# Optimization experiments

Measured on AMD Instinct MI355X. Metric: run time of the kernel, lower is better.

## Reference

```python
import jax, jax.numpy as jnp
import numpy as np

VOCAB = 32000; DIM = 512; NL = 6; B = 2; L = 1024
DI = 2 * DIM      # d_inner (expand=2)
DS = 16           # d_state
DC = 4            # d_conv
DR = DIM // 16    # dt_rank = ceil(512/16) = 32


def setup_inputs() -> dict:
    key = jax.random.key(0)
    ks = jax.random.split(key, 10)
    s = 0.02
    tokens = jax.random.randint(ks[0], (B, L), 0, VOCAB)
    pos_emb = jax.random.normal(ks[1], (1, L, DIM)) * s
    embed = jax.random.normal(ks[2], (VOCAB, DIM)) * s
    lm_w = jax.random.normal(ks[3], (VOCAB, DIM)) * s
    lm_b = jnp.zeros((VOCAB,), jnp.float32)
    in_proj_w = jax.random.normal(ks[4], (NL, 2 * DI, DIM)) * s
    conv_w = jax.random.normal(ks[5], (NL, DI, DC)) * s
    conv_b = jnp.zeros((NL, DI), jnp.float32)
    x_proj_w = jax.random.normal(ks[6], (NL, DR + 2 * DS, DI)) * s
    dt_proj_w = jax.random.normal(ks[7], (NL, DI, DR)) * s
    dt_proj_b = jnp.broadcast_to(jnp.log(jnp.expm1(jnp.float32(0.01))), (NL, DI)).astype(jnp.float32)
    A_log = jnp.log(jnp.broadcast_to(jnp.arange(1, DS + 1, dtype=jnp.float32), (NL, DI, DS)))
    Dp = jnp.ones((NL, DI), jnp.float32)
    out_w = jax.random.normal(ks[8], (NL, DIM, DI)) * s
    ln_g = jnp.ones((NL, DIM), jnp.float32)
    ln_b = jnp.zeros((NL, DIM), jnp.float32)
    return dict(tokens=tokens, pos_emb=pos_emb, embed=embed, lm_w=lm_w, lm_b=lm_b,
                in_proj_w=in_proj_w, conv_w=conv_w, conv_b=conv_b, x_proj_w=x_proj_w,
                dt_proj_w=dt_proj_w, dt_proj_b=dt_proj_b, A_log=A_log, Dp=Dp,
                out_w=out_w, ln_g=ln_g, ln_b=ln_b)


def silu(x):
    return x * jax.nn.sigmoid(x)


def layernorm(x, g, b, eps=1e-5):
    mu = jnp.mean(x, -1, keepdims=True)
    var = jnp.var(x, -1, keepdims=True)
    return (x - mu) * jax.lax.rsqrt(var + eps) * g + b


def causal_dwconv(x, w, b):
    # x: (B,L,DI), w: (DI,DC) depthwise, left-pad causal
    xp = jnp.pad(x, ((0, 0), (DC - 1, 0), (0, 0)))
    y = b
    for k in range(DC):
        y = y + w[:, k] * xp[:, k:k + x.shape[1], :]
    return y


def selective_scan(u, dt, A, Bm, Cm, Dp):
    # u,dt: (B,L,DI); A: (DI,DS); Bm,Cm: (B,L,DS)
    dA = jnp.exp(dt[..., None] * A)                       # (B,L,DI,DS)
    dBu = dt[..., None] * Bm[:, :, None, :] * u[..., None]
    h0 = jnp.zeros((u.shape[0], DI, DS), u.dtype)

    def step(h, inp):
        dA_t, dBu_t, C_t = inp
        h = dA_t * h + dBu_t
        y = jnp.einsum('bdn,bn->bd', h, C_t)
        return h, y

    _, ys = jax.lax.scan(step, h0, (dA.transpose(1, 0, 2, 3),
                                    dBu.transpose(1, 0, 2, 3),
                                    Cm.transpose(1, 0, 2)))
    return ys.transpose(1, 0, 2) + u * Dp


def mamba_block(x, in_w, cw, cb, xp_w, dtw, dtb, A_log, Dp, ow):
    xz = jnp.einsum('bld,ed->ble', x, in_w)               # (B,L,2*DI)
    xc, z = jnp.split(xz, 2, axis=-1)
    xc = silu(causal_dwconv(xc, cw, cb))
    x_dbl = jnp.einsum('bld,ed->ble', xc, xp_w)           # (B,L,DR+2*DS)
    dt, Bm, Cm = jnp.split(x_dbl, [DR, DR + DS], axis=-1)
    dt = jax.nn.softplus(jnp.einsum('blr,dr->bld', dt, dtw) + dtb)
    A = -jnp.exp(A_log)
    y = selective_scan(xc, dt, A, Bm, Cm, Dp)
    y = y * silu(z)
    return jnp.einsum('bld,ed->ble', y, ow)


def reference(tokens, pos_emb, embed, lm_w, lm_b, in_proj_w, conv_w, conv_b,
              x_proj_w, dt_proj_w, dt_proj_b, A_log, Dp, out_w, ln_g, ln_b):
    x = embed[tokens] + pos_emb[:, :tokens.shape[1]]
    for i in range(NL):
        res = x
        x = mamba_block(x, in_proj_w[i], conv_w[i], conv_b[i], x_proj_w[i],
                        dt_proj_w[i], dt_proj_b[i], A_log[i], Dp[i], out_w[i])
        x = layernorm(x + res, ln_g[i], ln_b[i])
    return jnp.einsum('bld,vd->blv', x, lm_w) + lm_b
```

## Files before the change

### kernel.cpp

```cpp
#include <hip/hip_runtime.h>
#include <hip/hip_bf16.h>
#include <math.h>

#define BB 2
#define LL 1024
#define DIM 512
#define NL 6
#define DI 1024
#define DS 16
#define DC 4
#define DR 32
#define VOCAB 32000
#define M_ROWS (BB * LL)
#define CCH 64
#define CHLEN (LL / CCH)
#define KSPLIT 8
#define OSPLIT 4

typedef unsigned short u16;
typedef __attribute__((ext_vector_type(8))) short bf16x8;
typedef __attribute__((ext_vector_type(4))) float f32x4;

__device__ __forceinline__ u16 f2bf(float f) {
    unsigned u = __float_as_uint(f);
    u += 0x7FFF + ((u >> 16) & 1);
    return (u16)(u >> 16);
}
__device__ __forceinline__ float bf2f(u16 h) {
    return __uint_as_float(((unsigned)h) << 16);
}
#define SWZ(r, c) ((c) ^ (((r) >> 1) & 3))

__global__ __launch_bounds__(256) void cast_all(const float* __restrict__ lm,
                                                const float* __restrict__ inw,
                                                const float* __restrict__ ow,
                                                const float* __restrict__ xp,
                                                u16* __restrict__ lmb,
                                                u16* __restrict__ inb,
                                                u16* __restrict__ owb_,
                                                u16* __restrict__ xpb) {
    int idx = blockIdx.x * 256 + threadIdx.x;
    const float* src; u16* dst; int off;
    if (idx < 2048000)      { src = lm;  dst = lmb;  off = idx; }
    else if (idx < 2834432) { src = inw; dst = inb;  off = idx - 2048000; }
    else if (idx < 3227648) { src = ow;  dst = owb_; off = idx - 2834432; }
    else                    { src = xp;  dst = xpb;  off = idx - 3227648; }
    float4 v0 = ((const float4*)src)[off * 2];
    float4 v1 = ((const float4*)src)[off * 2 + 1];
    union { u16 h[8]; int4 v; } r;
    r.h[0] = f2bf(v0.x); r.h[1] = f2bf(v0.y); r.h[2] = f2bf(v0.z); r.h[3] = f2bf(v0.w);
    r.h[4] = f2bf(v1.x); r.h[5] = f2bf(v1.y); r.h[6] = f2bf(v1.z); r.h[7] = f2bf(v1.w);
    ((int4*)dst)[off] = r.v;
}

__global__ __launch_bounds__(256) void embed_kernel(const int* __restrict__ tok,
                                                    const float* __restrict__ pos,
                                                    const float* __restrict__ emb,
                                                    float* __restrict__ x,
                                                    u16* __restrict__ xb) {
    int idx = blockIdx.x * 256 + threadIdx.x;
    int d = idx & (DIM - 1);
    int l = (idx >> 9) & (LL - 1);
    int b = idx >> 19;
    int t = tok[b * LL + l];
    float v = emb[(size_t)t * DIM + d] + pos[l * DIM + d];
    x[idx] = v;
    xb[idx] = f2bf(v);
}

__global__ __launch_bounds__(256) void gemm_n64(const u16* __restrict__ A,
                                                const u16* __restrict__ W,
                                                float* __restrict__ out,
                                                u16* __restrict__ outb,
                                                const float* __restrict__ bias,
                                                int lda, int ldw, int ldc,
                                                int KS, int pstride) {
    __shared__ __align__(16) char smem_raw[24576];
    u16* As = (u16*)smem_raw;
    u16* Ws = (u16*)(smem_raw + 16384);
    float* Cs = (float*)smem_raw;

    const int t = threadIdx.x;
    const int l = t & 63;
    const int w = t >> 6;
    const int gx = gridDim.x, gy = gridDim.y;
    const int nwg = gx * gy * gridDim.z;
    const int fid = (blockIdx.z * gy + blockIdx.y) * gx + blockIdx.x;
    const int q8 = nwg >> 3, r8 = nwg & 7;
    const int xcd = fid & 7, rank = fid >> 3;
    const int wgid = (xcd < r8 ? xcd * (q8 + 1) : r8 * (q8 + 1) + (xcd - r8) * q8) + rank;
    const int kz = wgid % gx;
    const int bm = ((wgid / gx) % gy) * 128;
    const int bnn = (wgid / (gx * gy)) * 64;
    const int wm = w * 32;

    f32x4 acc[2][4] = {};
    const int nt = KS >> 5;
    const int kbeg = kz * KS;

    auto STAGE = [&](int bufi, int k0) {
#pragma unroll
        for (int p = 0; p < 2; ++p) {
            const int i = p * 256 + w * 64 + l;
            const int row = i >> 2;
            const int kq = SWZ(row, i & 3);
            __builtin_amdgcn_global_load_lds(
                (const __attribute__((address_space(1))) unsigned int*)
                    (A + (size_t)(bm + row) * lda + k0 + kq * 8),
                (__attribute__((address_space(3))) unsigned int*)
                    (As + bufi * 4096 + (p * 256 + w * 64) * 8),
                16, 0, 0);
        }
        {
            const int i = w * 64 + l;
            const int row = i >> 2;
            const int kq = SWZ(row, i & 3);
            __builtin_amdgcn_global_load_lds(
                (const __attribute__((address_space(1))) unsigned int*)
                    (W + (size_t)(bnn + row) * ldw + k0 + kq * 8),
                (__attribute__((address_space(3))) unsigned int*)
                    (Ws + bufi * 2048 + (w * 64) * 8),
                16, 0, 0);
        }
    };
    auto COMPUTE = [&](int bufi) {
        const u16* Ab = As + bufi * 4096;
        const u16* Wb = Ws + bufi * 2048;
        bf16x8 bfr[4];
#pragma unroll
        for (int ni = 0; ni < 4; ++ni) {
            const int wr = ni * 16 + (l & 15);
            bfr[ni] = *(const bf16x8*)(Wb + wr * 32 + SWZ(wr, l >> 4) * 8);
        }
#pragma unroll
        for (int mi = 0; mi < 2; ++mi) {
            const int ar = wm + mi * 16 + (l & 15);
            bf16x8 a = *(const bf16x8*)(Ab + ar * 32 + SWZ(ar, l >> 4) * 8);
#pragma unroll
            for (int ni = 0; ni < 4; ++ni)
                acc[mi][ni] = __builtin_amdgcn_mfma_f32_16x16x32_bf16(bfr[ni], a, acc[mi][ni], 0, 0, 0);
        }
    };

    STAGE(0, kbeg);
    for (int tt = 0; tt < nt; ++tt) {
        if (tt + 1 < nt) {
            STAGE((tt + 1) & 1, kbeg + ((tt + 1) << 5));
            asm volatile("s_waitcnt vmcnt(3)\ns_barrier" ::: "memory");
        } else {
            asm volatile("s_waitcnt vmcnt(0)\ns_barrier" ::: "memory");
        }
        COMPUTE(tt & 1);
        asm volatile("s_waitcnt lgkmcnt(0)\ns_barrier" ::: "memory");
    }

    if (outb != nullptr) {
        u16* opb = outb + (size_t)kz * pstride;
#pragma unroll
        for (int mi = 0; mi < 2; ++mi) {
            const int row = bm + wm + mi * 16 + (l & 15);
#pragma unroll
            for (int ni = 0; ni < 4; ++ni) {
                const int col = bnn + ni * 16 + ((l >> 4) << 2);
                ushort4 v;
                v.x = f2bf(acc[mi][ni][0]); v.y = f2bf(acc[mi][ni][1]);
                v.z = f2bf(acc[mi][ni][2]); v.w = f2bf(acc[mi][ni][3]);
                *(ushort4*)(opb + (size_t)row * ldc + col) = v;
            }
        }
    } else {
        float* op = out + (size_t)kz * pstride;
#pragma unroll
        for (int pass = 0; pass < 2; ++pass) {
            if ((w >> 1) == pass) {
                const int rbase = (w & 1) * 32;
#pragma unroll
                for (int mi = 0; mi < 2; ++mi) {
                    const int r = rbase + mi * 16 + (l & 15);
#pragma unroll
                    for (int ni = 0; ni < 4; ++ni) {
                        const int c = ni * 16 + ((l >> 4) << 2);
                        float4 v;
                        v.x = acc[mi][ni][0]; v.y = acc[mi][ni][1];
                        v.z = acc[mi][ni][2]; v.w = acc[mi][ni][3];
                        *(float4*)(Cs + r * 65 + c) = v;
                    }
                }
            }
            __syncthreads();
#pragma unroll
            for (int it = 0; it < 4; ++it) {
                const int idx = it * 256 + t;
                const int r = idx >> 4;
                const int c4 = (idx & 15) * 4;
                float4 v = *(float4*)(Cs + r * 65 + c4);
                if (bias != nullptr) {
                    float4 b4 = *(const float4*)(bias + bnn + c4);
                    v.x += b4.x; v.y += b4.y; v.z += b4.z; v.w += b4.w;
                }
                *(float4*)(op + (size_t)(bm + pass * 64 + r) * ldc + bnn + c4) = v;
            }
            __syncthreads();
        }
    }
}

__global__ __launch_bounds__(256) void conv_silu(const u16* __restrict__ xzb,
                                                 const float* __restrict__ cw,
                                                 const float* __restrict__ cb,
                                                 u16* __restrict__ xcb) {
    int idx8 = blockIdx.x * 256 + threadIdx.x;
    int c0 = (idx8 & 127) * 8;
    int m = idx8 >> 7;
    int l = m & (LL - 1);

    float acc[8];
    float4 cb0 = *(const float4*)(cb + c0);
    float4 cb1 = *(const float4*)(cb + c0 + 4);
    acc[0] = cb0.x; acc[1] = cb0.y; acc[2] = cb0.z; acc[3] = cb0.w;
    acc[4] = cb1.x; acc[5] = cb1.y; acc[6] = cb1.z; acc[7] = cb1.w;
#pragma unroll
    for (int k = 0; k < DC; ++k) {
        int ll = l + k - (DC - 1);
        if (ll < 0) continue;
        const u16* row = xzb + ((size_t)(m + k - (DC - 1))) * (2 * DI) + c0;
        ushort4 r0 = *(const ushort4*)row;
        ushort4 r1 = *(const ushort4*)(row + 4);
#pragma unroll
        for (int j = 0; j < 4; ++j) {
            acc[j]     += cw[(c0 + j) * DC + k]     * bf2f(((const u16*)&r0)[j]);
            acc[j + 4] += cw[(c0 + j + 4) * DC + k] * bf2f(((const u16*)&r1)[j]);
        }
    }
    ushort4 o0, o1;
#pragma unroll
    for (int j = 0; j < 4; ++j) {
        float v0 = acc[j]     / (1.f + __expf(-acc[j]));
        float v1 = acc[j + 4] / (1.f + __expf(-acc[j + 4]));
        ((u16*)&o0)[j] = f2bf(v0);
        ((u16*)&o1)[j] = f2bf(v1);
    }
    u16* op = xcb + (size_t)idx8 * 8;
    *(ushort4*)op = o0;
    *(ushort4*)(op + 4) = o1;
}

__global__ __launch_bounds__(256) void scan_pass1(const u16* __restrict__ xcb,
                                                  const float* __restrict__ Pf,
                                                  const float* __restrict__ dtw,
                                                  const float* __restrict__ dtb,
                                                  const float* __restrict__ A_log,
                                                  float* __restrict__ S,
                                                  float* __restrict__ Q) {
    __shared__ float xds[CHLEN][64];
    const int t = threadIdx.x;
    const int d = blockIdx.x * 256 + t;
    const int b = blockIdx.y;
    const int c = blockIdx.z;
    const int l0 = c * CHLEN;
    const int m0 = b * LL + l0;

    for (int i = t; i < CHLEN * 64; i += 256) {
        int r = i >> 6, cc = i & 63;
        float s = 0.f;
#pragma unroll
        for (int kz = 0; kz < KSPLIT; ++kz)
            s += Pf[(size_t)kz * (M_ROWS * 64) + (m0 + r) * 64 + cc];
        xds[r][cc] = s;
    }
    __syncthreads();

    float4 wreg[8];
#pragma unroll
    for (int kk = 0; kk < 8; ++kk)
        wreg[kk] = *(const float4*)(dtw + (size_t)d * DR + kk * 4);
    const float dtbv = dtb[d];

    float a[DS];
#pragma unroll
    for (int q = 0; q < 4; ++q) {
        float4 al = *(const float4*)(A_log + d * DS + q * 4);
        a[q * 4 + 0] = -__expf(al.x);
        a[q * 4 + 1] = -__expf(al.y);
        a[q * 4 + 2] = -__expf(al.z);
        a[q * 4 + 3] = -__expf(al.w);
    }
    float Qr[DS];
#pragma unroll
    for (int n = 0; n < DS; ++n) Qr[n] = 0.f;
    float Ssum = 0.f;

    const u16* up = xcb + (size_t)m0 * DI + d;

    for (int l = 0; l < CHLEN; ++l) {
        float dacc = dtbv;
#pragma unroll
        for (int kk = 0; kk < 8; ++kk) {
            float4 xv = *(const float4*)&xds[l][kk * 4];
            dacc += wreg[kk].x * xv.x + wreg[kk].y * xv.y +
                    wreg[kk].z * xv.z + wreg[kk].w * xv.w;
        }
        float dtv = (dacc > 20.f) ? dacc : log1pf(__expf(dacc));
        float uv = bf2f(up[(size_t)l * DI]);
        float wv = dtv * uv;
        Ssum += dtv;
#pragma unroll
        for (int q = 0; q < 4; ++q) {
            float4 Bv = *(const float4*)&xds[l][32 + q * 4];
            float dA0 = __expf(dtv * a[q * 4 + 0]);
            float dA1 = __expf(dtv * a[q * 4 + 1]);
            float dA2 = __expf(dtv * a[q * 4 + 2]);
            float dA3 = __expf(dtv * a[q * 4 + 3]);
            Qr[q * 4 + 0] = dA0 * Qr[q * 4 + 0] + wv * Bv.x;
            Qr[q * 4 + 1] = dA1 * Qr[q * 4 + 1] + wv * Bv.y;
            Qr[q * 4 + 2] = dA2 * Qr[q * 4 + 2] + wv * Bv.z;
            Qr[q * 4 + 3] = dA3 * Qr[q * 4 + 3] + wv * Bv.w;
        }
    }
    S[((size_t)b * CCH + c) * DI + d] = Ssum;
    float* Qp = Q + (((size_t)b * CCH + c) * DI + d) * DS;
#pragma unroll
    for (int q = 0; q < 4; ++q) {
        float4 o;
        o.x = Qr[q * 4 + 0]; o.y = Qr[q * 4 + 1];
        o.z = Qr[q * 4 + 2]; o.w = Qr[q * 4 + 3];
        *(float4*)(Qp + q * 4) = o;
    }
}

__global__ __launch_bounds__(64) void scan_pass2(const float* __restrict__ A_log,
                                                 const float* __restrict__ S,
                                                 float* __restrict__ Q) {
    const int idx = blockIdx.x * 64 + threadIdx.x;
    const int b = idx >> 14;
    const int dn = idx & 16383;
    const int d = dn >> 4;
    const float a = -__expf(A_log[dn]);
    float h = 0.f;
    for (int c = 0; c < CCH; ++c) {
        const size_t soff = ((size_t)b * CCH + c) * DI + d;
        const size_t qoff = ((size_t)b * CCH + c) * (size_t)(DI * DS) + dn;
        float P = __expf(a * S[soff]);
        float qv = Q[qoff];
        Q[qoff] = h;
        h = P * h + qv;
    }
}

__global__ __launch_bounds__(256) void scan_pass3(const u16* __restrict__ xcb,
                                                  const float* __restrict__ Pf,
                                                  const float* __restrict__ dtw,
                                                  const float* __restrict__ dtb,
                                                  const u16* __restrict__ xzb,
                                                  const float* __restrict__ A_log,
                                                  const float* __restrict__ Dpp,
                                                  const float* __restrict__ Q,
                                                  u16* __restrict__ y) {
    __shared__ float xds[CHLEN][64];
    const int t = threadIdx.x;
    const int d = blockIdx.x * 256 + t;
    const int b = blockIdx.y;
    const int c = blockIdx.z;
    const int l0 = c * CHLEN;
    const int m0 = b * LL + l0;

    for (int i = t; i < CHLEN * 64; i += 256) {
        int r = i >> 6, cc = i & 63;
        float s = 0.f;
#pragma unroll
        for (int kz = 0; kz < KSPLIT; ++kz)
            s += Pf[(size_t)kz * (M_ROWS * 64) + (m0 + r) * 64 + cc];
        xds[r][cc] = s;
    }
    __syncthreads();

    float4 wreg[8];
#pragma unroll
    for (int kk = 0; kk < 8; ++kk)
        wreg[kk] = *(const float4*)(dtw + (size_t)d * DR + kk * 4);
    const float dtbv = dtb[d];

    float a[DS];
#pragma unroll
    for (int q = 0; q < 4; ++q) {
        float4 al = *(const float4*)(A_log + d * DS + q * 4);
        a[q * 4 + 0] = -__expf(al.x);
        a[q * 4 + 1] = -__expf(al.y);
        a[q * 4 + 2] = -__expf(al.z);
        a[q * 4 + 3] = -__expf(al.w);
    }
    float h[DS];
    const float* Qp = Q + (((size_t)b * CCH + c) * DI + d) * DS;
#pragma unroll
    for (int q = 0; q < 4; ++q) {
        float4 hv = *(const float4*)(Qp + q * 4);
        h[q * 4 + 0] = hv.x; h[q * 4 + 1] = hv.y;
        h[q * 4 + 2] = hv.z; h[q * 4 + 3] = hv.w;
    }
    const float dp = Dpp[d];

    const u16* up = xcb + (size_t)m0 * DI + d;
    const u16* zp = xzb + (size_t)m0 * (2 * DI) + DI + d;
    u16* yp = y + (size_t)m0 * DI + d;

    for (int l = 0; l < CHLEN; ++l) {
        float dacc = dtbv;
#pragma unroll
        for (int kk = 0; kk < 8; ++kk) {
            float4 xv = *(const float4*)&xds[l][kk * 4];
            dacc += wreg[kk].x * xv.x + wreg[kk].y * xv.y +
                    wreg[kk].z * xv.z + wreg[kk].w * xv.w;
        }
        float dtv = (dacc > 20.f) ? dacc : log1pf(__expf(dacc));
        float uv = bf2f(up[(size_t)l * DI]);
        float wv = dtv * uv;
        float p = 0.f;
#pragma unroll
        for (int q = 0; q < 4; ++q) {
            float4 Bv = *(const float4*)&xds[l][32 + q * 4];
            float4 Cv = *(const float4*)&xds[l][48 + q * 4];
            float dA0 = __expf(dtv * a[q * 4 + 0]);
            float dA1 = __expf(dtv * a[q * 4 + 1]);
            float dA2 = __expf(dtv * a[q * 4 + 2]);
            float dA3 = __expf(dtv * a[q * 4 + 3]);
            h[q * 4 + 0] = dA0 * h[q * 4 + 0] + wv * Bv.x;
            h[q * 4 + 1] = dA1 * h[q * 4 + 1] + wv * Bv.y;
            h[q * 4 + 2] = dA2 * h[q * 4 + 2] + wv * Bv.z;
            h[q * 4 + 3] = dA3 * h[q * 4 + 3] + wv * Bv.w;
            p += h[q * 4 + 0] * Cv.x + h[q * 4 + 1] * Cv.y +
                 h[q * 4 + 2] * Cv.z + h[q * 4 + 3] * Cv.w;
        }
        float zv = bf2f(zp[(size_t)l * (2 * DI)]);
        float g = zv / (1.f + __expf(-zv));
        yp[(size_t)l * DI] = f2bf((p + uv * dp) * g);
    }
}

__global__ __launch_bounds__(256) void add_ln(const float* __restrict__ opart,
                                              float* __restrict__ x,
                                              const float* __restrict__ g,
                                              const float* __restrict__ b,
                                              u16* __restrict__ xb) {
    const int PS = M_ROWS * DIM;
    int m = blockIdx.x;
    int t = threadIdx.x;
    const float* xr = x + (size_t)m * DIM;
    float v0 = xr[t];
    float v1 = xr[t + 256];
#pragma unroll
    for (int kz = 0; kz < OSPLIT; ++kz) {
        const float* op = opart + (size_t)kz * PS + (size_t)m * DIM;
        v0 += op[t];
        v1 += op[t + 256];
    }
    float s = v0 + v1;
    float ss = v0 * v0 + v1 * v1;
#pragma unroll
    for (int off = 32; off > 0; off >>= 1) {
        s += __shfl_down(s, off, 64);
        ss += __shfl_down(ss, off, 64);
    }
    __shared__ float sb[4], ssb[4];
    int w = t >> 6;
    if ((t & 63) == 0) { sb[w] = s; ssb[w] = ss; }
    __syncthreads();
    float stot = sb[0] + sb[1] + sb[2] + sb[3];
    float sstot = ssb[0] + ssb[1] + ssb[2] + ssb[3];
    float mean = stot * (1.f / DIM);
    float var = sstot * (1.f / DIM) - mean * mean;
    float rs = rsqrtf(var + 1e-5f);
    float* xw = x + (size_t)m * DIM;
    float o0 = (v0 - mean) * rs * g[t] + b[t];
    float o1 = (v1 - mean) * rs * g[t + 256] + b[t + 256];
    xw[t] = o0;
    xw[t + 256] = o1;
    xb[(size_t)m * DIM + t] = f2bf(o0);
    xb[(size_t)m * DIM + t + 256] = f2bf(o1);
}

extern "C" void kernel_launch(void* const* d_in, const int* in_sizes, int n_in,
                              void* d_out, int out_size, void* d_ws, size_t ws_size,
                              hipStream_t stream) {
    const int*   tokens = (const int*)d_in[0];
    const float* pos    = (const float*)d_in[1];
    const float* emb    = (const float*)d_in[2];
    const float* lm_w   = (const float*)d_in[3];
    const float* lm_b   = (const float*)d_in[4];
    const float* in_w   = (const float*)d_in[5];
    const float* cw     = (const float*)d_in[6];
    const float* cb     = (const float*)d_in[7];
    const float* xpw    = (const float*)d_in[8];
    const float* dtw    = (const float*)d_in[9];
    const float* dtb    = (const float*)d_in[10];
    const float* A_log  = (const float*)d_in[11];
    const float* Dpp    = (const float*)d_in[12];
    const float* ow     = (const float*)d_in[13];
    const float* lng    = (const float*)d_in[14];
    const float* lnb    = (const float*)d_in[15];
    float* out = (float*)d_out;

    float* ws = (float*)d_ws;
    float* x    = ws;
    float* S    = x + 1048576;
    float* Qb   = S + 131072;
    float* Pf   = Qb + 2097152;
    float* Pf2  = Pf + 1048576;
    u16* xzb    = (u16*)(Pf2 + 4194304);
    u16* xb     = xzb + 4194304;
    u16* yb     = xb + 1048576;
    u16* xcb    = yb + 2097152;
    u16* lm_wb  = xcb + 2097152;
    u16* in_wb  = lm_wb + 16384000;
    u16* owb    = in_wb + 6291456;
    u16* xpwb   = owb + 3145728;

    cast_all<<<12800, 256, 0, stream>>>(lm_w, in_w, ow, xpw,
                                        lm_wb, in_wb, owb, xpwb);

    embed_kernel<<<M_ROWS * DIM / 256, 256, 0, stream>>>(tokens, pos, emb, x, xb);

    for (int i = 0; i < NL; ++i) {
        gemm_n64<<<dim3(1, M_ROWS / 128, 2048 / 64), 256, 0, stream>>>(
            xb, in_wb + (size_t)i * 2048 * 512, nullptr, xzb, nullptr,
            512, 512, 2048, 512, 0);
        conv_silu<<<M_ROWS * DI / 8 / 256, 256, 0, stream>>>(
            xzb, cw + (size_t)i * DI * DC, cb + (size_t)i * DI, xcb);
        gemm_n64<<<dim3(KSPLIT, M_ROWS / 128, 1), 256, 0, stream>>>(
            xcb, xpwb + (size_t)i * 64 * 1024, Pf, nullptr, nullptr,
            1024, 1024, 64, 1024 / KSPLIT, M_ROWS * 64);
        scan_pass1<<<dim3(DI / 256, BB, CCH), 256, 0, stream>>>(
            xcb, Pf, dtw + (size_t)i * DI * DR, dtb + (size_t)i * DI,
            A_log + (size_t)i * DI * DS, S, Qb);
        scan_pass2<<<(BB * DI * DS) / 64, 64, 0, stream>>>(
            A_log + (size_t)i * DI * DS, S, Qb);
        scan_pass3<<<dim3(DI / 256, BB, CCH), 256, 0, stream>>>(
            xcb, Pf, dtw + (size_t)i * DI * DR, dtb + (size_t)i * DI, xzb,
            A_log + (size_t)i * DI * DS, Dpp + (size_t)i * DI, Qb, yb);
        gemm_n64<<<dim3(OSPLIT, M_ROWS / 128, 512 / 64), 256, 0, stream>>>(
            yb, owb + (size_t)i * 512 * 1024, Pf2, nullptr, nullptr,
            1024, 1024, 512, 1024 / OSPLIT, M_ROWS * 512);
        add_ln<<<M_ROWS, 256, 0, stream>>>(
            Pf2, x, lng + (size_t)i * DIM, lnb + (size_t)i * DIM, xb);
    }

    gemm_n64<<<dim3(1, M_ROWS / 128, VOCAB / 64), 256, 0, stream>>>(
        xb, lm_wb, out, nullptr, lm_b,
        512, 512, VOCAB, 512, 0);
}
```

Measured before the change: 851.0 us.

## Fuse three-pass chunked scan into one kernel with decoupled look-back

Merges the scan's three kernels (per-chunk local scan, cross-chunk prefix, and output pass) into one kernel. Each chunk block publishes its local state and dt sum, then walks back through earlier chunks using per-chain epoch flags until it finds a published inclusive state, in the style of decoupled look-back. This removes two launches, the serial pass-2 kernel and the recomputation of the dt projection and Pf reduction in the third pass. In exchange it adds spin-waiting on flags, which relies on blocks being scheduled in forward progress order, plus atomic reads from global memory.

```diff
diff --git a/kernel.cpp b/kernel.cpp
--- a/kernel.cpp
+++ b/kernel.cpp
@@ -245,18 +245,27 @@
     *(ushort4*)(op + 4) = o1;
 }
 
-__global__ __launch_bounds__(256) void scan_pass1(const u16* __restrict__ xcb,
+__global__ __launch_bounds__(256) void scan_fused(const u16* __restrict__ xcb,
                                                   const float* __restrict__ Pf,
                                                   const float* __restrict__ dtw,
                                                   const float* __restrict__ dtb,
+                                                  const u16* __restrict__ xzb,
                                                   const float* __restrict__ A_log,
-                                                  float* __restrict__ S,
-                                                  float* __restrict__ Q) {
+                                                  const float* __restrict__ Dpp,
+                                                  float* Spub,
+                                                  float* Qpub,
+                                                  float* Hpub,
+                                                  int* flags,
+                                                  int ep1,
+                                                  u16* __restrict__ y) {
     __shared__ float xds[CHLEN][64];
+    __shared__ int sflag;
     const int t = threadIdx.x;
     const int d = blockIdx.x * 256 + t;
     const int b = blockIdx.y;
     const int c = blockIdx.z;
+    const int chain = blockIdx.x * BB + b;
+    const int ep2 = ep1 + 1;
     const int l0 = c * CHLEN;
     const int m0 = b * LL + l0;
 
@@ -285,11 +294,11 @@
         a[q * 4 + 2] = -__expf(al.z);
         a[q * 4 + 3] = -__expf(al.w);
     }
+
     float Qr[DS];
 #pragma unroll
     for (int n = 0; n < DS; ++n) Qr[n] = 0.f;
     float Ssum = 0.f;
-
     const u16* up = xcb + (size_t)m0 * DI + d;
 
     for (int l = 0; l < CHLEN; ++l) {
@@ -305,101 +314,75 @@
         float wv = dtv * uv;
         Ssum += dtv;
 #pragma unroll
-        for (int q = 0; q < 4; ++q) {
-            float4 Bv = *(const float4*)&xds[l][32 + q * 4];
-            float dA0 = __expf(dtv * a[q * 4 + 0]);
-            float dA1 = __expf(dtv * a[q * 4 + 1]);
-            float dA2 = __expf(dtv * a[q * 4 + 2]);
-            float dA3 = __expf(dtv * a[q * 4 + 3]);
-            Qr[q * 4 + 0] = dA0 * Qr[q * 4 + 0] + wv * Bv.x;
-            Qr[q * 4 + 1] = dA1 * Qr[q * 4 + 1] + wv * Bv.y;
-            Qr[q * 4 + 2] = dA2 * Qr[q * 4 + 2] + wv * Bv.z;
-            Qr[q * 4 + 3] = dA3 * Qr[q * 4 + 3] + wv * Bv.w;
-        }
-    }
-    S[((size_t)b * CCH + c) * DI + d] = Ssum;
-    float* Qp = Q + (((size_t)b * CCH + c) * DI + d) * DS;
-#pragma unroll
-    for (int q = 0; q < 4; ++q) {
-        float4 o;
-        o.x = Qr[q * 4 + 0]; o.y = Qr[q * 4 + 1];
-        o.z = Qr[q * 4 + 2]; o.w = Qr[q * 4 + 3];
-        *(float4*)(Qp + q * 4) = o;
-    }
-}
-
-__global__ __launch_bounds__(64) void scan_pass2(const float* __restrict__ A_log,
-                                                 const float* __restrict__ S,
-                                                 float* __restrict__ Q) {
-    const int idx = blockIdx.x * 64 + threadIdx.x;
-    const int b = idx >> 14;
-    const int dn = idx & 16383;
-    const int d = dn >> 4;
-    const float a = -__expf(A_log[dn]);
-    float h = 0.f;
-    for (int c = 0; c < CCH; ++c) {
-        const size_t soff = ((size_t)b * CCH + c) * DI + d;
-        const size_t qoff = ((size_t)b * CCH + c) * (size_t)(DI * DS) + dn;
-        float P = __expf(a * S[soff]);
-        float qv = Q[qoff];
-        Q[qoff] = h;
-        h = P * h + qv;
-    }
-}
-
-__global__ __launch_bounds__(256) void scan_pass3(const u16* __restrict__ xcb,
-                                                  const float* __restrict__ Pf,
-                                                  const float* __restrict__ dtw,
-                                                  const float* __restrict__ dtb,
-                                                  const u16* __restrict__ xzb,
-                                                  const float* __restrict__ A_log,
-                                                  const float* __restrict__ Dpp,
-                                                  const float* __restrict__ Q,
-                                                  u16* __restrict__ y) {
-    __shared__ float xds[CHLEN][64];
-    const int t = threadIdx.x;
-    const int d = blockIdx.x * 256 + t;
-    const int b = blockIdx.y;
-    const int c = blockIdx.z;
-    const int l0 = c * CHLEN;
-    const int m0 = b * LL + l0;
-
-    for (int i = t; i < CHLEN * 64; i += 256) {
-        int r = i >> 6, cc = i & 63;
-        float s = 0.f;
-#pragma unroll
-        for (int kz = 0; kz < KSPLIT; ++kz)
-            s += Pf[(size_t)kz * (M_ROWS * 64) + (m0 + r) * 64 + cc];
-        xds[r][cc] = s;
-    }
+        for (int n = 0; n < DS; ++n) {
+            float Bv = xds[l][32 + n];
+            Qr[n] = __expf(dtv * a[n]) * Qr[n] + wv * Bv;
+        }
+    }
+
+    {
+        const size_t base = ((size_t)(b * CCH + c) * DS) * DI + d;
+#pragma unroll
+        for (int n = 0; n < DS; ++n) Qpub[base + (size_t)n * DI] = Qr[n];
+        Spub[(size_t)(b * CCH + c) * DI + d] = Ssum;
+    }
+    __threadfence();
     __syncthreads();
-
-    float4 wreg[8];
-#pragma unroll
-    for (int kk = 0; kk < 8; ++kk)
-        wreg[kk] = *(const float4*)(dtw + (size_t)d * DR + kk * 4);
-    const float dtbv = dtb[d];
-
-    float a[DS];
-#pragma unroll
-    for (int q = 0; q < 4; ++q) {
-        float4 al = *(const float4*)(A_log + d * DS + q * 4);
-        a[q * 4 + 0] = -__expf(al.x);
-        a[q * 4 + 1] = -__expf(al.y);
-        a[q * 4 + 2] = -__expf(al.z);
-        a[q * 4 + 3] = -__expf(al.w);
-    }
+    if (t == 0) atomicExch(&flags[chain * CCH + c], ep1);
+
     float h[DS];
-    const float* Qp = Q + (((size_t)b * CCH + c) * DI + d) * DS;
-#pragma unroll
-    for (int q = 0; q < 4; ++q) {
-        float4 hv = *(const float4*)(Qp + q * 4);
-        h[q * 4 + 0] = hv.x; h[q * 4 + 1] = hv.y;
-        h[q * 4 + 2] = hv.z; h[q * 4 + 3] = hv.w;
-    }
+#pragma unroll
+    for (int n = 0; n < DS; ++n) h[n] = 0.f;
+    float Sacc = 0.f;
+
+    if (c > 0) {
+        int k = c - 1;
+        while (true) {
+            if (t == 0) {
+                int v;
+                do {
+                    v = atomicAdd(&flags[chain * CCH + k], 0);
+                    if (v < ep1) __builtin_amdgcn_s_sleep(2);
+                } while (v < ep1);
+                sflag = v;
+            }
+            __syncthreads();
+            const int v = sflag;
+            __syncthreads();
+            if (v >= ep2) {
+                const size_t base = ((size_t)(b * CCH + k) * DS) * DI + d;
+#pragma unroll
+                for (int n = 0; n < DS; ++n) {
+                    float hv = atomicAdd(&Hpub[base + (size_t)n * DI], 0.f);
+                    h[n] += __expf(a[n] * Sacc) * hv;
+                }
+                break;
+            } else {
+                const size_t base = ((size_t)(b * CCH + k) * DS) * DI + d;
+#pragma unroll
+                for (int n = 0; n < DS; ++n) {
+                    float qv = atomicAdd(&Qpub[base + (size_t)n * DI], 0.f);
+                    h[n] += __expf(a[n] * Sacc) * qv;
+                }
+                float Sk = atomicAdd(&Spub[(size_t)(b * CCH + k) * DI + d], 0.f);
+                Sacc += Sk;
+                if (k == 0) break;
+                --k;
+            }
+        }
+    }
+
+    {
+        const size_t base = ((size_t)(b * CCH + c) * DS) * DI + d;
+#pragma unroll
+        for (int n = 0; n < DS; ++n)
+            Hpub[base + (size_t)n * DI] = Qr[n] + __expf(a[n] * Ssum) * h[n];
+    }
+    __threadfence();
+    __syncthreads();
+    if (t == 0) atomicExch(&flags[chain * CCH + c], ep2);
+
     const float dp = Dpp[d];
-
-    const u16* up = xcb + (size_t)m0 * DI + d;
     const u16* zp = xzb + (size_t)m0 * (2 * DI) + DI + d;
     u16* yp = y + (size_t)m0 * DI + d;
 
@@ -416,19 +399,11 @@
         float wv = dtv * uv;
         float p = 0.f;
 #pragma unroll
-        for (int q = 0; q < 4; ++q) {
-            float4 Bv = *(const float4*)&xds[l][32 + q * 4];
-            float4 Cv = *(const float4*)&xds[l][48 + q * 4];
-            float dA0 = __expf(dtv * a[q * 4 + 0]);
-            float dA1 = __expf(dtv * a[q * 4 + 1]);
-            float dA2 = __expf(dtv * a[q * 4 + 2]);
-            float dA3 = __expf(dtv * a[q * 4 + 3]);
-            h[q * 4 + 0] = dA0 * h[q * 4 + 0] + wv * Bv.x;
-            h[q * 4 + 1] = dA1 * h[q * 4 + 1] + wv * Bv.y;
-            h[q * 4 + 2] = dA2 * h[q * 4 + 2] + wv * Bv.z;
-            h[q * 4 + 3] = dA3 * h[q * 4 + 3] + wv * Bv.w;
-            p += h[q * 4 + 0] * Cv.x + h[q * 4 + 1] * Cv.y +
-                 h[q * 4 + 2] * Cv.z + h[q * 4 + 3] * Cv.w;
+        for (int n = 0; n < DS; ++n) {
+            float Bv = xds[l][32 + n];
+            float Cv = xds[l][48 + n];
+            h[n] = __expf(dtv * a[n]) * h[n] + wv * Bv;
+            p += h[n] * Cv;
         }
         float zv = bf2f(zp[(size_t)l * (2 * DI)]);
         float g = zv / (1.f + __expf(-zv));
@@ -501,11 +476,13 @@
 
     float* ws = (float*)d_ws;
     float* x    = ws;
-    float* S    = x + 1048576;
-    float* Qb   = S + 131072;
-    float* Pf   = Qb + 2097152;
+    float* Spub = x + 1048576;
+    float* Qpub = Spub + 131072;
+    float* Hpub = Qpub + 2097152;
+    float* Pf   = Hpub + 2097152;
     float* Pf2  = Pf + 1048576;
-    u16* xzb    = (u16*)(Pf2 + 4194304);
+    int*  flags = (int*)(Pf2 + 4194304);
+    u16* xzb    = (u16*)((float*)flags + 1024);
     u16* xb     = xzb + 4194304;
     u16* yb     = xb + 1048576;
     u16* xcb    = yb + 2097152;
@@ -513,6 +490,8 @@
     u16* in_wb  = lm_wb + 16384000;
     u16* owb    = in_wb + 6291456;
     u16* xpwb   = owb + 3145728;
+
+    hipMemsetAsync(flags, 0, 512 * sizeof(int), stream);
 
     cast_all<<<12800, 256, 0, stream>>>(lm_w, in_w, ow, xpw,
                                         lm_wb, in_wb, owb, xpwb);
@@ -528,14 +507,10 @@
         gemm_n64<<<dim3(KSPLIT, M_ROWS / 128, 1), 256, 0, stream>>>(
             xcb, xpwb + (size_t)i * 64 * 1024, Pf, nullptr, nullptr,
             1024, 1024, 64, 1024 / KSPLIT, M_ROWS * 64);
-        scan_pass1<<<dim3(DI / 256, BB, CCH), 256, 0, stream>>>(
-            xcb, Pf, dtw + (size_t)i * DI * DR, dtb + (size_t)i * DI,
-            A_log + (size_t)i * DI * DS, S, Qb);
-        scan_pass2<<<(BB * DI * DS) / 64, 64, 0, stream>>>(
-            A_log + (size_t)i * DI * DS, S, Qb);
-        scan_pass3<<<dim3(DI / 256, BB, CCH), 256, 0, stream>>>(
+        scan_fused<<<dim3(DI / 256, BB, CCH), 256, 0, stream>>>(
             xcb, Pf, dtw + (size_t)i * DI * DR, dtb + (size_t)i * DI, xzb,
-            A_log + (size_t)i * DI * DS, Dpp + (size_t)i * DI, Qb, yb);
+            A_log + (size_t)i * DI * DS, Dpp + (size_t)i * DI,
+            Spub, Qpub, Hpub, flags, 2 * i + 1, yb);
         gemm_n64<<<dim3(OSPLIT, M_ROWS / 128, 512 / 64), 256, 0, stream>>>(
             yb, owb + (size_t)i * 512 * 1024, Pf2, nullptr, nullptr,
             1024, 1024, 512, 1024 / OSPLIT, M_ROWS * 512);
```

New measurement: 1.553 ms. 82.5% more time.
